# Kernel tuning notes

Measured on AMD Instinct MI355X. Metric: run time of the kernel, lower is better.

The kernel has to match this reference:

```python
import jax, jax.numpy as jnp
import numpy as np

EPS = 1e-12
B, S, H, NH, L, F = 8, 512, 768, 12, 12, 3072
V, TV, P = 21128, 2, 512
DH = H // NH


def layer_norm(x, g, b):
    m = jnp.mean(x, axis=-1, keepdims=True)
    v = jnp.var(x, axis=-1, keepdims=True)
    return g * (x - m) / jnp.sqrt(v + EPS) + b


def setup_inputs() -> dict:
    key = jax.random.key(0)
    ks = iter(jax.random.split(key, 40))
    r = lambda shape: (jax.random.normal(next(ks), shape, jnp.float32) * 0.02)
    inp = {
        "input_ids": jax.random.randint(next(ks), (B, S), 0, V, jnp.int32),
        "segment_ids": jax.random.randint(next(ks), (B, S), 0, TV, jnp.int32),
        "attention_mask": jnp.ones((B, 1, 1, S), jnp.float32),
        "tok_emb": r((V, H)),
        "pos_emb": r((P, H)),
        "type_emb": r((TV, H)),
        "emb_g": jnp.ones((H,), jnp.float32),
        "emb_b": jnp.zeros((H,), jnp.float32),
        # stacked per-layer params [L, ...]
        "Wq": r((L, H, H)), "bq": jnp.zeros((L, H), jnp.float32),
        "Wk": r((L, H, H)), "bk": jnp.zeros((L, H), jnp.float32),
        "Wv": r((L, H, H)), "bv": jnp.zeros((L, H), jnp.float32),
        "Wao": r((L, H, H)), "bao": jnp.zeros((L, H), jnp.float32),
        "ln1_g": jnp.ones((L, H), jnp.float32), "ln1_b": jnp.zeros((L, H), jnp.float32),
        "Wi": r((L, H, F)), "bi": jnp.zeros((L, F), jnp.float32),
        "Wio": r((L, F, H)), "bio": jnp.zeros((L, H), jnp.float32),
        "ln2_g": jnp.ones((L, H), jnp.float32), "ln2_b": jnp.zeros((L, H), jnp.float32),
    }
    return inp


def reference(input_ids, segment_ids, attention_mask,
              tok_emb, pos_emb, type_emb, emb_g, emb_b,
              Wq, bq, Wk, bk, Wv, bv, Wao, bao, ln1_g, ln1_b,
              Wi, bi, Wio, bio, ln2_g, ln2_b):
    # ---- embedding: token + type + position, then LayerNorm ----
    x = tok_emb[input_ids] + type_emb[segment_ids] + pos_emb[None, :S, :]
    x = layer_norm(x, emb_g, emb_b)  # [B,S,H]

    mask_add = (1.0 - attention_mask) * -10000.0  # [B,1,1,S]
    scale = 1.0 / jnp.sqrt(jnp.asarray(DH, x.dtype))

    def split_heads(t):  # [B,S,H] -> [B,NH,S,DH]
        return t.reshape(B, S, NH, DH).transpose(0, 2, 1, 3)

    for l in range(Wq.shape[0]):
        q = split_heads(x @ Wq[l] + bq[l])
        k = split_heads(x @ Wk[l] + bk[l])
        v = split_heads(x @ Wv[l] + bv[l])
        score = jnp.einsum("bhqd,bhkd->bhqk", q, k) * scale + mask_add
        attn = jax.nn.softmax(score, axis=-1)
        ctx = jnp.einsum("bhqk,bhkd->bhqd", attn, v)
        ctx = ctx.transpose(0, 2, 1, 3).reshape(B, S, H)
        # attention output: dense + residual + LN
        attn_out = layer_norm(ctx @ Wao[l] + bao[l] + x, ln1_g[l], ln1_b[l])
        # FFN: dense-gelu-dense + residual + LN (exact erf gelu as in tf.keras)
        h = jax.nn.gelu(attn_out @ Wi[l] + bi[l], approximate=False)
        x = layer_norm(h @ Wio[l] + bio[l] + attn_out, ln2_g[l], ln2_b[l])

    return x  # sequence output [B,S,H]
```

## Files before the change

kernel.cpp:

```cpp
#include <hip/hip_runtime.h>
#include <math.h>

static constexpr int Bc = 8;
static constexpr int Sc = 512;
static constexpr int Hc = 768;
static constexpr int NHc = 12;
static constexpr int Lc = 12;
static constexpr int Fc = 3072;
static constexpr int DHc = 64;
static constexpr int NTOK = Bc * Sc;
static constexpr int QKVN = 3 * Hc;

static constexpr size_t W_QKV_OFF = 0;
static constexpr size_t W_AO_OFF  = 1769472;
static constexpr size_t W_I_OFF   = 2359296;
static constexpr size_t W_IO_OFF  = 4718592;
static constexpr size_t LW        = 7077888;

typedef _Float16 h16x8 __attribute__((ext_vector_type(8)));
typedef float f32x4 __attribute__((ext_vector_type(4)));
typedef unsigned short us4 __attribute__((ext_vector_type(4)));
typedef unsigned int u32x4 __attribute__((ext_vector_type(4)));

__device__ __forceinline__ unsigned short f2h(float f) {
    _Float16 h = (_Float16)f;
    return __builtin_bit_cast(unsigned short, h);
}

#define AS1 __attribute__((address_space(1)))
#define AS3 __attribute__((address_space(3)))
__device__ __forceinline__ void gld_lds16(const void* g, void* l) {
    __builtin_amdgcn_global_load_lds((const AS1 void*)g, (AS3 void*)l, 16, 0, 0);
}

__global__ __launch_bounds__(256) void prep_kernel(
    const float* __restrict__ Wq, const float* __restrict__ Wk,
    const float* __restrict__ Wv, const float* __restrict__ Wao,
    const float* __restrict__ Wi, const float* __restrict__ Wio,
    const float* __restrict__ bq, const float* __restrict__ bk,
    const float* __restrict__ bv, unsigned short* __restrict__ WALL,
    float* __restrict__ BALL)
{
    int t = blockIdx.x, l = blockIdx.y;
    int tid = threadIdx.x;

    if (t >= 6912) {
        int idx = (t - 6912) * 256 + tid;
        float v = (idx < 768) ? bq[l * Hc + idx]
                : (idx < 1536) ? bk[l * Hc + idx - 768]
                               : bv[l * Hc + idx - 1536];
        BALL[(size_t)l * QKVN + idx] = v;
        return;
    }

    const float* src;
    unsigned short* dst;
    int K, N, ntn, local;
    if (t < 2304) {
        int mat = t / 576; local = t % 576;
        K = 768; N = 768; ntn = 24;
        src = (mat == 0 ? Wq : mat == 1 ? Wk : mat == 2 ? Wv : Wao) + (size_t)l * 589824;
        dst = WALL + (size_t)l * LW + (mat < 3 ? (size_t)mat * 589824 : W_AO_OFF);
    } else if (t < 4608) {
        local = t - 2304; K = 768; N = 3072; ntn = 96;
        src = Wi + (size_t)l * 2359296;
        dst = WALL + (size_t)l * LW + W_I_OFF;
    } else {
        local = t - 4608; K = 3072; N = 768; ntn = 24;
        src = Wio + (size_t)l * 2359296;
        dst = WALL + (size_t)l * LW + W_IO_OFF;
    }
    int n0 = (local % ntn) * 32, k0 = (local / ntn) * 32;
    int tx = tid & 31, ty = tid >> 5;

    __shared__ float tl[32][33];
#pragma unroll
    for (int j = 0; j < 4; j++)
        tl[ty + j * 8][tx] = src[(size_t)(k0 + ty + j * 8) * N + n0 + tx];
    __syncthreads();
#pragma unroll
    for (int j = 0; j < 4; j++)
        dst[(size_t)(n0 + ty + j * 8) * K + k0 + tx] = f2h(tl[tx][ty + j * 8]);
}

__global__ __launch_bounds__(256) void embed_ln_kernel(
    const int* __restrict__ ids, const int* __restrict__ seg,
    const float* __restrict__ tok, const float* __restrict__ typ,
    const float* __restrict__ pos, const float* __restrict__ g,
    const float* __restrict__ b, float* __restrict__ outf,
    unsigned short* __restrict__ outb)
{
    int t = blockIdx.x;
    int si = t % Sc;
    int id = ids[t], sg = seg[t];
    const float* tp = tok + (size_t)id * Hc;
    const float* yp = typ + (size_t)sg * Hc;
    const float* pp = pos + (size_t)si * Hc;

    float e[3];
    float s = 0.f, s2 = 0.f;
#pragma unroll
    for (int j = 0; j < 3; j++) {
        int h = threadIdx.x + j * 256;
        float v = tp[h] + yp[h] + pp[h];
        e[j] = v; s += v; s2 += v * v;
    }
    __shared__ float red[8];
#pragma unroll
    for (int o = 32; o > 0; o >>= 1) { s += __shfl_xor(s, o); s2 += __shfl_xor(s2, o); }
    int lane = threadIdx.x & 63, wid = threadIdx.x >> 6;
    if (lane == 0) { red[wid] = s; red[4 + wid] = s2; }
    __syncthreads();
    if (threadIdx.x == 0) {
        red[0] = red[0] + red[1] + red[2] + red[3];
        red[4] = red[4] + red[5] + red[6] + red[7];
    }
    __syncthreads();
    float mean = red[0] * (1.0f / Hc);
    float var  = red[4] * (1.0f / Hc) - mean * mean;
    float rstd = rsqrtf(var + 1e-12f);
    float* op = outf + (size_t)t * Hc;
    unsigned short* ob = outb + (size_t)t * Hc;
#pragma unroll
    for (int j = 0; j < 3; j++) {
        int h = threadIdx.x + j * 256;
        float v = g[h] * (e[j] - mean) * rstd + b[h];
        op[h] = v;
        ob[h] = f2h(v);
    }
}

__global__ __launch_bounds__(256) void add_ln_kernel(
    const unsigned short* __restrict__ tin, const float* __restrict__ res,
    const float* __restrict__ g, const float* __restrict__ b,
    float* __restrict__ outf, unsigned short* __restrict__ outb)
{
    int t = blockIdx.x;
    const unsigned short* ip = tin + (size_t)t * Hc;
    const float* rp = res + (size_t)t * Hc;

    float e[3];
    float s = 0.f, s2 = 0.f;
#pragma unroll
    for (int j = 0; j < 3; j++) {
        int h = threadIdx.x + j * 256;
        float v = (float)__builtin_bit_cast(_Float16, ip[h]) + rp[h];
        e[j] = v; s += v; s2 += v * v;
    }
    __shared__ float red[8];
#pragma unroll
    for (int o = 32; o > 0; o >>= 1) { s += __shfl_xor(s, o); s2 += __shfl_xor(s2, o); }
    int lane = threadIdx.x & 63, wid = threadIdx.x >> 6;
    if (lane == 0) { red[wid] = s; red[4 + wid] = s2; }
    __syncthreads();
    if (threadIdx.x == 0) {
        red[0] = red[0] + red[1] + red[2] + red[3];
        red[4] = red[4] + red[5] + red[6] + red[7];
    }
    __syncthreads();
    float mean = red[0] * (1.0f / Hc);
    float var  = red[4] * (1.0f / Hc) - mean * mean;
    float rstd = rsqrtf(var + 1e-12f);
    float* op = outf + (size_t)t * Hc;
    unsigned short* ob = outb + (size_t)t * Hc;
#pragma unroll
    for (int j = 0; j < 3; j++) {
        int h = threadIdx.x + j * 256;
        float v = g[h] * (e[j] - mean) * rstd + b[h];
        op[h] = v;
        ob[h] = f2h(v);
    }
}

template <int OUT>
__global__ __launch_bounds__(256) void gemm_mfma(
    const unsigned short* __restrict__ A,
    const unsigned short* __restrict__ Bt,
    const float* __restrict__ bias,
    unsigned short* __restrict__ Cb,
    unsigned short* __restrict__ VTp,
    int M, int N, int K)
{
    __shared__ __align__(16) unsigned short As[128 * 64];
    __shared__ __align__(16) unsigned short Bs[128 * 64];

    int tid = threadIdx.x;
    int l = tid & 63, w = tid >> 6;
    int m0 = blockIdx.x * 128, n0 = blockIdx.y * 128;
    int lr = l & 15;
    int kg = l >> 4;
    int wr = (w >> 1) * 64, wc = (w & 1) * 64;
    int lx = lr & 7;

    f32x4 acc[4][4] = {};

    for (int k0 = 0; k0 < K; k0 += 64) {
#pragma unroll
        for (int p = 0; p < 4; p++) {
            int i = p * 256 + w * 64 + l;
            int row = i >> 3;
            int slot = (i & 7) ^ (row & 7);
            const unsigned short* ga = A + (size_t)(m0 + row) * K + k0 + slot * 8;
            const unsigned short* gb = Bt + (size_t)(n0 + row) * K + k0 + slot * 8;
            unsigned short* la = As + (size_t)(p * 256 + w * 64) * 8;
            unsigned short* lb = Bs + (size_t)(p * 256 + w * 64) * 8;
            gld_lds16(ga, la);
            gld_lds16(gb, lb);
        }
        asm volatile("s_waitcnt vmcnt(0)" ::: "memory");
        __syncthreads();

#pragma unroll
        for (int kh = 0; kh < 2; kh++) {
            h16x8 av[4], bv[4];
#pragma unroll
            for (int f = 0; f < 4; f++) {
                int sl = (kh * 4 + kg) ^ lx;
                av[f] = *(const h16x8*)(As + (wr + f * 16 + lr) * 64 + sl * 8);
                bv[f] = *(const h16x8*)(Bs + (wc + f * 16 + lr) * 64 + sl * 8);
            }
#pragma unroll
            for (int i = 0; i < 4; i++)
#pragma unroll
                for (int j = 0; j < 4; j++)
                    acc[i][j] = __builtin_amdgcn_mfma_f32_16x16x32_f16(
                        av[i], bv[j], acc[i][j], 0, 0, 0);
        }
        __syncthreads();
    }

#pragma unroll
    for (int i = 0; i < 4; i++) {
        int rbase = m0 + wr + i * 16 + kg * 4;
#pragma unroll
        for (int j = 0; j < 4; j++) {
            int col = n0 + wc + j * 16 + lr;
            float bcol = bias[col];
            if (OUT == 3 && col >= 1536) {
                int vcol = col - 1536;
                int hh = vcol >> 6, d = vcol & 63;
                int bbb = rbase >> 9, s0 = rbase & 511;
                us4 ob;
#pragma unroll
                for (int r = 0; r < 4; r++) ob[r] = f2h(acc[i][j][r] + bcol);
                *(us4*)(VTp + ((((size_t)bbb * NHc + hh) * DHc + d) << 9) + s0) = ob;
            } else {
                int ldc = (OUT == 3) ? 1536 : N;
#pragma unroll
                for (int r = 0; r < 4; r++) {
                    float v = acc[i][j][r] + bcol;
                    if (OUT == 1) v = 0.5f * v * (1.0f + erff(v * 0.70710678118654752f));
                    Cb[(size_t)(rbase + r) * ldc + col] = f2h(v);
                }
            }
        }
    }
}

__global__ __launch_bounds__(256) void attn_mfma(
    const unsigned short* __restrict__ QK, const unsigned short* __restrict__ VT,
    const float* __restrict__ mask, unsigned short* __restrict__ O)
{
    const int LD = 1536;
    __shared__ __align__(16) unsigned short Ks[64 * 64];
    __shared__ __align__(16) unsigned short Vt[64 * 64];
    __shared__ float Ml[64];

    int tid = threadIdx.x;
    int l = tid & 63, w = tid >> 6;
    int g = l >> 4, c = l & 15;
    int q0 = blockIdx.x * 64;
    int h = blockIdx.y, bb = blockIdx.z;

    const size_t rowQ = (size_t)(bb * Sc + q0 + w * 16 + c) * LD + h * DHc;
    h16x8 qv[2];
    qv[0] = *(const h16x8*)(QK + rowQ + 8 * g);
    qv[1] = *(const h16x8*)(QK + rowQ + 32 + 8 * g);

    float m_run = -1e30f, l_run = 0.f;
    f32x4 acc_o[4] = {};
    const float scale = 0.125f;

    for (int kt = 0; kt < Sc; kt += 64) {
        const unsigned short* Kgb = QK + (size_t)(bb * Sc + kt) * LD + Hc + h * DHc;
#pragma unroll
        for (int p = 0; p < 2; p++) {
            int i = p * 256 + tid;
            int row = i >> 3;
            int slot = (i & 7) ^ (row & 7);
            gld_lds16(Kgb + (size_t)row * LD + slot * 8, Ks + (size_t)(p * 256 + w * 64) * 8);
        }
        const unsigned short* Vg = VT + (((size_t)bb * NHc + h) * DHc << 9) + kt;
#pragma unroll
        for (int p = 0; p < 2; p++) {
            int i = p * 256 + tid;
            int row = i >> 3;
            int slot = (i & 7) ^ (row & 7);
            gld_lds16(Vg + ((size_t)row << 9) + slot * 8, Vt + (size_t)(p * 256 + w * 64) * 8);
        }
        if (tid < 64) Ml[tid] = (1.0f - mask[bb * Sc + kt + tid]) * -10000.0f;
        asm volatile("s_waitcnt vmcnt(0)" ::: "memory");
        __syncthreads();

        f32x4 s[4] = {};
#pragma unroll
        for (int kh = 0; kh < 2; kh++) {
#pragma unroll
            for (int f = 0; f < 4; f++) {
                int row = f * 16 + c;
                h16x8 av = *(const h16x8*)(Ks + row * 64 + (((kh * 4 + g) ^ (row & 7)) * 8));
                s[f] = __builtin_amdgcn_mfma_f32_16x16x32_f16(av, qv[kh], s[f], 0, 0, 0);
            }
        }

        f32x4 mv[4];
#pragma unroll
        for (int f = 0; f < 4; f++) mv[f] = *(const f32x4*)&Ml[f * 16 + 4 * g];
        float mx = -1e30f;
#pragma unroll
        for (int f = 0; f < 4; f++)
#pragma unroll
            for (int r = 0; r < 4; r++) {
                float sv = s[f][r] * scale + mv[f][r];
                s[f][r] = sv;
                mx = fmaxf(mx, sv);
            }
        mx = fmaxf(mx, __shfl_xor(mx, 16));
        mx = fmaxf(mx, __shfl_xor(mx, 32));
        float mn = fmaxf(m_run, mx);
        float fs = __expf(m_run - mn);
        m_run = mn;
        float ps = 0.f;
        f32x4 p[4];
#pragma unroll
        for (int f = 0; f < 4; f++)
#pragma unroll
            for (int r = 0; r < 4; r++) {
                float pv = __expf(s[f][r] - mn);
                p[f][r] = pv;
                ps += pv;
            }
        ps += __shfl_xor(ps, 16);
        ps += __shfl_xor(ps, 32);
        l_run = l_run * fs + ps;
#pragma unroll
        for (int fm = 0; fm < 4; fm++)
#pragma unroll
            for (int r = 0; r < 4; r++) acc_o[fm][r] *= fs;

        unsigned pk[4][2];
#pragma unroll
        for (int f = 0; f < 4; f++)
#pragma unroll
            for (int rp = 0; rp < 2; rp++)
                pk[f][rp] = ((unsigned)f2h(p[f][2 * rp + 1]) << 16) | f2h(p[f][2 * rp]);

#pragma unroll
        for (int kh = 0; kh < 2; kh++) {
            u32x4 bw;
#pragma unroll
            for (int t = 0; t < 4; t++) {
                int srcl = (2 * ((l >> 4) & 1) + (t >> 1)) * 16 + c;
                unsigned lo = __shfl(pk[2 * kh][t & 1], srcl);
                unsigned hi = __shfl(pk[2 * kh + 1][t & 1], srcl);
                bw[t] = (g & 2) ? hi : lo;
            }
            h16x8 bfrag = __builtin_bit_cast(h16x8, bw);
#pragma unroll
            for (int fm = 0; fm < 4; fm++) {
                int row = fm * 16 + c;
                h16x8 av = *(const h16x8*)(Vt + row * 64 + (((kh * 4 + g) ^ (row & 7)) * 8));
                acc_o[fm] = __builtin_amdgcn_mfma_f32_16x16x32_f16(av, bfrag, acc_o[fm], 0, 0, 0);
            }
        }
        __syncthreads();
    }

    float rl = 1.0f / l_run;
    size_t tokrow = (size_t)(bb * Sc + q0 + w * 16 + c) * Hc + h * DHc;
#pragma unroll
    for (int fm = 0; fm < 4; fm++) {
        us4 ob;
#pragma unroll
        for (int r = 0; r < 4; r++) ob[r] = f2h(acc_o[fm][r] * rl);
        *(us4*)(O + tokrow + fm * 16 + 4 * g) = ob;
    }
}

extern "C" void kernel_launch(void* const* d_in, const int* in_sizes, int n_in,
                              void* d_out, int out_size, void* d_ws, size_t ws_size,
                              hipStream_t stream)
{
    const int*   input_ids      = (const int*)  d_in[0];
    const int*   segment_ids    = (const int*)  d_in[1];
    const float* attention_mask = (const float*)d_in[2];
    const float* tok_emb = (const float*)d_in[3];
    const float* pos_emb = (const float*)d_in[4];
    const float* type_emb= (const float*)d_in[5];
    const float* emb_g   = (const float*)d_in[6];
    const float* emb_b   = (const float*)d_in[7];
    const float* Wq  = (const float*)d_in[8];  const float* bq  = (const float*)d_in[9];
    const float* Wk  = (const float*)d_in[10]; const float* bk  = (const float*)d_in[11];
    const float* Wv  = (const float*)d_in[12]; const float* bv  = (const float*)d_in[13];
    const float* Wao = (const float*)d_in[14]; const float* bao = (const float*)d_in[15];
    const float* ln1_g = (const float*)d_in[16]; const float* ln1_b = (const float*)d_in[17];
    const float* Wi  = (const float*)d_in[18]; const float* bi  = (const float*)d_in[19];
    const float* Wio = (const float*)d_in[20]; const float* bio = (const float*)d_in[21];
    const float* ln2_g = (const float*)d_in[22]; const float* ln2_b = (const float*)d_in[23];

    float* out = (float*)d_out;

    const size_t NT = (size_t)NTOK * Hc;
    float* Xf   = (float*)d_ws;
    float* XAf  = Xf + NT;
    float* BALL = XAf + NT;
    unsigned short* QKb = (unsigned short*)(BALL + (size_t)Lc * QKVN);
    unsigned short* VT  = QKb + (size_t)NTOK * 1536;
    unsigned short* Xb  = VT + NT;
    unsigned short* XAb = Xb + NT;
    unsigned short* Cb  = XAb + NT;
    unsigned short* Tb  = Cb + NT;
    unsigned short* Hb  = Tb + NT;
    unsigned short* WALL = Hb + (size_t)NTOK * Fc;

    prep_kernel<<<dim3(6921, Lc), 256, 0, stream>>>(Wq, Wk, Wv, Wao, Wi, Wio,
                                                    bq, bk, bv, WALL, BALL);

    embed_ln_kernel<<<NTOK, 256, 0, stream>>>(input_ids, segment_ids, tok_emb,
                                              type_emb, pos_emb, emb_g, emb_b, Xf, Xb);

    dim3 gQKV(NTOK / 128, QKVN / 128);
    dim3 gH(NTOK / 128, Hc / 128);
    dim3 gF(NTOK / 128, Fc / 128);
    dim3 gA(Sc / 64, NHc, Bc);

    for (int l = 0; l < Lc; l++) {
        const unsigned short* WqkvT = WALL + (size_t)l * LW + W_QKV_OFF;
        const unsigned short* WaoT  = WALL + (size_t)l * LW + W_AO_OFF;
        const unsigned short* WiT   = WALL + (size_t)l * LW + W_I_OFF;
        const unsigned short* WioT  = WALL + (size_t)l * LW + W_IO_OFF;
        const float* bqkv = BALL + (size_t)l * QKVN;

        gemm_mfma<3><<<gQKV, 256, 0, stream>>>(Xb, WqkvT, bqkv, QKb, VT,
                                               NTOK, QKVN, Hc);
        attn_mfma<<<gA, 256, 0, stream>>>(QKb, VT, attention_mask, Cb);

        gemm_mfma<2><<<gH, 256, 0, stream>>>(Cb, WaoT, bao + (size_t)l * Hc, Tb, nullptr,
                                             NTOK, Hc, Hc);
        add_ln_kernel<<<NTOK, 256, 0, stream>>>(Tb, Xf, ln1_g + (size_t)l * Hc,
                                                ln1_b + (size_t)l * Hc, XAf, XAb);

        gemm_mfma<1><<<gF, 256, 0, stream>>>(XAb, WiT, bi + (size_t)l * Fc, Hb, nullptr,
                                             NTOK, Fc, Hc);
        gemm_mfma<2><<<gH, 256, 0, stream>>>(Hb, WioT, bio + (size_t)l * Hc, Tb, nullptr,
                                             NTOK, Hc, Fc);
        float* xout = (l == Lc - 1) ? out : Xf;
        add_ln_kernel<<<NTOK, 256, 0, stream>>>(Tb, XAf, ln2_g + (size_t)l * Hc,
                                                ln2_b + (size_t)l * Hc, xout, Xb);
    }
}
```

Baseline: 2.363 ms.

## Split-K the FFN output GEMM and fuse partial-sum reduction into LayerNorm

The FFN down-projection (K=3072, N=768) only launched 192 blocks, so it is now split along K into two halves across blockIdx.z. Each half writes fp32 partials, which a new add_ln2f kernel sums with the residual before LayerNorm. This also keeps the pre-LN sum in fp32 rather than fp16. Separately, the weight transpose/convert prep kernel now uses 64x64 tiles with float4 loads and 16-byte stores. The price is extra fp32 traffic for the two partial buffers.

Result: faster. 2.070 ms (-12.4%).

```diff
diff --git a/kernel.cpp b/kernel.cpp
--- a/kernel.cpp
+++ b/kernel.cpp
@@ -20,6 +20,7 @@
 typedef _Float16 h16x8 __attribute__((ext_vector_type(8)));
 typedef float f32x4 __attribute__((ext_vector_type(4)));
 typedef unsigned short us4 __attribute__((ext_vector_type(4)));
+typedef unsigned short us8 __attribute__((ext_vector_type(8)));
 typedef unsigned int u32x4 __attribute__((ext_vector_type(4)));
 
 __device__ __forceinline__ unsigned short f2h(float f) {
@@ -44,8 +45,8 @@
     int t = blockIdx.x, l = blockIdx.y;
     int tid = threadIdx.x;
 
-    if (t >= 6912) {
-        int idx = (t - 6912) * 256 + tid;
+    if (t >= 1728) {
+        int idx = (t - 1728) * 256 + tid;
         float v = (idx < 768) ? bq[l * Hc + idx]
                 : (idx < 1536) ? bk[l * Hc + idx - 768]
                                : bv[l * Hc + idx - 1536];
@@ -56,31 +57,41 @@
     const float* src;
     unsigned short* dst;
     int K, N, ntn, local;
-    if (t < 2304) {
-        int mat = t / 576; local = t % 576;
-        K = 768; N = 768; ntn = 24;
+    if (t < 576) {
+        int mat = t / 144; local = t % 144;
+        K = 768; N = 768; ntn = 12;
         src = (mat == 0 ? Wq : mat == 1 ? Wk : mat == 2 ? Wv : Wao) + (size_t)l * 589824;
         dst = WALL + (size_t)l * LW + (mat < 3 ? (size_t)mat * 589824 : W_AO_OFF);
-    } else if (t < 4608) {
-        local = t - 2304; K = 768; N = 3072; ntn = 96;
+    } else if (t < 1152) {
+        local = t - 576; K = 768; N = 3072; ntn = 48;
         src = Wi + (size_t)l * 2359296;
         dst = WALL + (size_t)l * LW + W_I_OFF;
     } else {
-        local = t - 4608; K = 3072; N = 768; ntn = 24;
+        local = t - 1152; K = 3072; N = 768; ntn = 12;
         src = Wio + (size_t)l * 2359296;
         dst = WALL + (size_t)l * LW + W_IO_OFF;
     }
-    int n0 = (local % ntn) * 32, k0 = (local / ntn) * 32;
-    int tx = tid & 31, ty = tid >> 5;
-
-    __shared__ float tl[32][33];
-#pragma unroll
-    for (int j = 0; j < 4; j++)
-        tl[ty + j * 8][tx] = src[(size_t)(k0 + ty + j * 8) * N + n0 + tx];
-    __syncthreads();
-#pragma unroll
-    for (int j = 0; j < 4; j++)
-        dst[(size_t)(n0 + ty + j * 8) * K + k0 + tx] = f2h(tl[tx][ty + j * 8]);
+    int n0 = (local % ntn) * 64, k0 = (local / ntn) * 64;
+
+    __shared__ float tl[64][65];
+    int tx = tid & 15, ty = tid >> 4;
+#pragma unroll
+    for (int j = 0; j < 4; j++) {
+        int k = ty + j * 16;
+        float4 v = *(const float4*)(src + (size_t)(k0 + k) * N + n0 + tx * 4);
+        tl[k][tx * 4 + 0] = v.x; tl[k][tx * 4 + 1] = v.y;
+        tl[k][tx * 4 + 2] = v.z; tl[k][tx * 4 + 3] = v.w;
+    }
+    __syncthreads();
+#pragma unroll
+    for (int q = 0; q < 2; q++) {
+        int chunk = q * 256 + tid;
+        int row = chunk >> 3, c = chunk & 7;
+        us8 o;
+#pragma unroll
+        for (int j = 0; j < 8; j++) o[j] = f2h(tl[c * 8 + j][row]);
+        *(us8*)(dst + (size_t)(n0 + row) * K + k0 + c * 8) = o;
+    }
 }
 
 __global__ __launch_bounds__(256) void embed_ln_kernel(
@@ -145,6 +156,50 @@
     for (int j = 0; j < 3; j++) {
         int h = threadIdx.x + j * 256;
         float v = (float)__builtin_bit_cast(_Float16, ip[h]) + rp[h];
+        e[j] = v; s += v; s2 += v * v;
+    }
+    __shared__ float red[8];
+#pragma unroll
+    for (int o = 32; o > 0; o >>= 1) { s += __shfl_xor(s, o); s2 += __shfl_xor(s2, o); }
+    int lane = threadIdx.x & 63, wid = threadIdx.x >> 6;
+    if (lane == 0) { red[wid] = s; red[4 + wid] = s2; }
+    __syncthreads();
+    if (threadIdx.x == 0) {
+        red[0] = red[0] + red[1] + red[2] + red[3];
+        red[4] = red[4] + red[5] + red[6] + red[7];
+    }
+    __syncthreads();
+    float mean = red[0] * (1.0f / Hc);
+    float var  = red[4] * (1.0f / Hc) - mean * mean;
+    float rstd = rsqrtf(var + 1e-12f);
+    float* op = outf + (size_t)t * Hc;
+    unsigned short* ob = outb + (size_t)t * Hc;
+#pragma unroll
+    for (int j = 0; j < 3; j++) {
+        int h = threadIdx.x + j * 256;
+        float v = g[h] * (e[j] - mean) * rstd + b[h];
+        op[h] = v;
+        ob[h] = f2h(v);
+    }
+}
+
+__global__ __launch_bounds__(256) void add_ln2f_kernel(
+    const float* __restrict__ t0, const float* __restrict__ t1,
+    const float* __restrict__ res, const float* __restrict__ g,
+    const float* __restrict__ b, float* __restrict__ outf,
+    unsigned short* __restrict__ outb)
+{
+    int t = blockIdx.x;
+    const float* i0 = t0 + (size_t)t * Hc;
+    const float* i1 = t1 + (size_t)t * Hc;
+    const float* rp = res + (size_t)t * Hc;
+
+    float e[3];
+    float s = 0.f, s2 = 0.f;
+#pragma unroll
+    for (int j = 0; j < 3; j++) {
+        int h = threadIdx.x + j * 256;
+        float v = i0[h] + i1[h] + rp[h];
         e[j] = v; s += v; s2 += v * v;
     }
     __shared__ float red[8];
@@ -179,7 +234,8 @@
     const float* __restrict__ bias,
     unsigned short* __restrict__ Cb,
     unsigned short* __restrict__ VTp,
-    int M, int N, int K)
+    float* __restrict__ Cf,
+    int M, int N, int K, int kspan)
 {
     __shared__ __align__(16) unsigned short As[128 * 64];
     __shared__ __align__(16) unsigned short Bs[128 * 64];
@@ -191,10 +247,11 @@
     int kg = l >> 4;
     int wr = (w >> 1) * 64, wc = (w & 1) * 64;
     int lx = lr & 7;
+    int kbeg = blockIdx.z * kspan;
 
     f32x4 acc[4][4] = {};
 
-    for (int k0 = 0; k0 < K; k0 += 64) {
+    for (int k0 = kbeg; k0 < kbeg + kspan; k0 += 64) {
 #pragma unroll
         for (int p = 0; p < 4; p++) {
             int i = p * 256 + w * 64 + l;
@@ -235,7 +292,7 @@
 #pragma unroll
         for (int j = 0; j < 4; j++) {
             int col = n0 + wc + j * 16 + lr;
-            float bcol = bias[col];
+            float bcol = (OUT == 4 && blockIdx.z > 0) ? 0.f : bias[col];
             if (OUT == 3 && col >= 1536) {
                 int vcol = col - 1536;
                 int hh = vcol >> 6, d = vcol & 63;
@@ -244,6 +301,11 @@
 #pragma unroll
                 for (int r = 0; r < 4; r++) ob[r] = f2h(acc[i][j][r] + bcol);
                 *(us4*)(VTp + ((((size_t)bbb * NHc + hh) * DHc + d) << 9) + s0) = ob;
+            } else if (OUT == 4) {
+                float* op = Cf + (size_t)blockIdx.z * M * N;
+#pragma unroll
+                for (int r = 0; r < 4; r++)
+                    op[(size_t)(rbase + r) * N + col] = acc[i][j][r] + bcol;
             } else {
                 int ldc = (OUT == 3) ? 1536 : N;
 #pragma unroll
@@ -413,7 +475,8 @@
     const size_t NT = (size_t)NTOK * Hc;
     float* Xf   = (float*)d_ws;
     float* XAf  = Xf + NT;
-    float* BALL = XAf + NT;
+    float* Tf01 = XAf + NT;
+    float* BALL = Tf01 + 2 * NT;
     unsigned short* QKb = (unsigned short*)(BALL + (size_t)Lc * QKVN);
     unsigned short* VT  = QKb + (size_t)NTOK * 1536;
     unsigned short* Xb  = VT + NT;
@@ -423,7 +486,7 @@
     unsigned short* Hb  = Tb + NT;
     unsigned short* WALL = Hb + (size_t)NTOK * Fc;
 
-    prep_kernel<<<dim3(6921, Lc), 256, 0, stream>>>(Wq, Wk, Wv, Wao, Wi, Wio,
+    prep_kernel<<<dim3(1737, Lc), 256, 0, stream>>>(Wq, Wk, Wv, Wao, Wi, Wio,
                                                     bq, bk, bv, WALL, BALL);
 
     embed_ln_kernel<<<NTOK, 256, 0, stream>>>(input_ids, segment_ids, tok_emb,
@@ -432,6 +495,7 @@
     dim3 gQKV(NTOK / 128, QKVN / 128);
     dim3 gH(NTOK / 128, Hc / 128);
     dim3 gF(NTOK / 128, Fc / 128);
+    dim3 gH2(NTOK / 128, Hc / 128, 2);
     dim3 gA(Sc / 64, NHc, Bc);
 
     for (int l = 0; l < Lc; l++) {
@@ -441,21 +505,22 @@
         const unsigned short* WioT  = WALL + (size_t)l * LW + W_IO_OFF;
         const float* bqkv = BALL + (size_t)l * QKVN;
 
-        gemm_mfma<3><<<gQKV, 256, 0, stream>>>(Xb, WqkvT, bqkv, QKb, VT,
-                                               NTOK, QKVN, Hc);
+        gemm_mfma<3><<<gQKV, 256, 0, stream>>>(Xb, WqkvT, bqkv, QKb, VT, nullptr,
+                                               NTOK, QKVN, Hc, Hc);
         attn_mfma<<<gA, 256, 0, stream>>>(QKb, VT, attention_mask, Cb);
 
         gemm_mfma<2><<<gH, 256, 0, stream>>>(Cb, WaoT, bao + (size_t)l * Hc, Tb, nullptr,
-                                             NTOK, Hc, Hc);
+                                             nullptr, NTOK, Hc, Hc, Hc);
         add_ln_kernel<<<NTOK, 256, 0, stream>>>(Tb, Xf, ln1_g + (size_t)l * Hc,
                                                 ln1_b + (size_t)l * Hc, XAf, XAb);
 
         gemm_mfma<1><<<gF, 256, 0, stream>>>(XAb, WiT, bi + (size_t)l * Fc, Hb, nullptr,
-                                             NTOK, Fc, Hc);
-        gemm_mfma<2><<<gH, 256, 0, stream>>>(Hb, WioT, bio + (size_t)l * Hc, Tb, nullptr,
-                                             NTOK, Hc, Fc);
+                                             nullptr, NTOK, Fc, Hc, Hc);
+        gemm_mfma<4><<<gH2, 256, 0, stream>>>(Hb, WioT, bio + (size_t)l * Hc, nullptr,
+                                              nullptr, Tf01, NTOK, Hc, Fc, Fc / 2);
         float* xout = (l == Lc - 1) ? out : Xf;
-        add_ln_kernel<<<NTOK, 256, 0, stream>>>(Tb, XAf, ln2_g + (size_t)l * Hc,
-                                                ln2_b + (size_t)l * Hc, xout, Xb);
-    }
-}
+        add_ln2f_kernel<<<NTOK, 256, 0, stream>>>(Tf01, Tf01 + NT, XAf,
+                                                  ln2_g + (size_t)l * Hc,
+                                                  ln2_b + (size_t)l * Hc, xout, Xb);
+    }
+}
```
